# Performance work log

Measured on AMD Instinct MI355X. Metric: run time of the kernel, lower is better.

## Reference

```python
import jax, jax.numpy as jnp
import numpy as np

B, NPTS = 2, 60000
NX, NY = 256, 256
PCR0, PCR1 = -32.0, -32.0
PS0, PS1 = 0.25, 0.25
MAXPP = 32      # max points per pillar
MAXP = 12000    # max pillars
C = 64          # lidar_channels
SENT = NX * NY  # sentinel pillar id (> any valid id)
NEG = -1e9
EPS = 1e-5


def setup_inputs():
    key = jax.random.key(0)
    ks = jax.random.split(key, 16)
    xy = jax.random.uniform(ks[0], (B, NPTS, 2), minval=-34.0, maxval=34.0)
    z = jax.random.uniform(ks[1], (B, NPTS, 1), minval=-3.0, maxval=1.0)
    ir = jax.random.uniform(ks[2], (B, NPTS, 2))
    pts = jnp.concatenate([xy, z, ir], axis=-1).astype(jnp.float32)
    mask = jax.random.uniform(ks[3], (B, NPTS)) < 0.98

    def lin(k, i, o):
        return (jax.random.normal(k, (i, o)) / np.sqrt(i)).astype(jnp.float32)

    inp = {"lidar_points": pts, "lidar_mask": mask,
           "w1": lin(ks[4], 10, 64), "b1": 0.01 * jax.random.normal(ks[5], (64,), jnp.float32),
           "g1": jnp.ones(64, jnp.float32), "be1": jnp.zeros(64, jnp.float32),
           "w2": lin(ks[6], 64, 64), "b2": 0.01 * jax.random.normal(ks[7], (64,), jnp.float32),
           "g2": jnp.ones(64, jnp.float32), "be2": jnp.zeros(64, jnp.float32)}
    for i, n in enumerate(["1", "2", "3"]):
        inp["cw" + n] = (jax.random.normal(ks[8 + i], (64, 64, 3, 3)) / np.sqrt(64 * 9)).astype(jnp.float32)
        inp["cb" + n] = 0.01 * jax.random.normal(ks[11 + i], (64,), jnp.float32)
        inp["cg" + n] = jnp.ones(64, jnp.float32)
        inp["cbe" + n] = jnp.zeros(64, jnp.float32)
    return inp


def bn1d(x, g, b):  # training-mode BN over rows (biased var), matches torch BatchNorm1d forward
    m = x.mean(0)
    v = ((x - m) ** 2).mean(0)
    return (x - m) * jax.lax.rsqrt(v + EPS) * g + b


def bn2d(x, g, b):  # training-mode BN over (N,H,W) per channel
    m = x.mean((0, 2, 3), keepdims=True)
    v = ((x - m) ** 2).mean((0, 2, 3), keepdims=True)
    return (x - m) * jax.lax.rsqrt(v + EPS) * g[None, :, None, None] + b[None, :, None, None]


def conv3(x, w, b):
    y = jax.lax.conv_general_dilated(x, w, (1, 1), 'SAME',
                                     dimension_numbers=('NCHW', 'OIHW', 'NCHW'))
    return y + b[None, :, None, None]


def pillarize(pts, msk):
    """pts: (N,5) xyzir, msk: (N,) bool -> padded pillar tensors (fixed shapes)."""
    n = pts.shape[0]
    ix = jnp.clip(((pts[:, 0] - PCR0) / PS0).astype(jnp.int32), 0, NX - 1)
    iy = jnp.clip(((pts[:, 1] - PCR1) / PS1).astype(jnp.int32), 0, NY - 1)
    pid = jnp.where(msk, iy * NX + ix, SENT)
    # sorted unique ids; keep the first (smallest) MAXP, like torch.unique + truncation
    spid = jnp.sort(pid)
    is_new = jnp.concatenate([jnp.array([True]), spid[1:] != spid[:-1]])
    urank = jnp.cumsum(is_new) - 1
    dest = jnp.where(is_new & (urank < MAXP) & (spid < SENT), urank, MAXP)
    uids = jnp.full((MAXP + 1,), SENT, dtype=pid.dtype).at[dest].set(spid)[:MAXP]  # ascending, SENT-padded
    inv = jnp.clip(jnp.searchsorted(uids, pid), 0, MAXP - 1)
    valid = (uids[inv] == pid) & (pid < SENT)
    # rank of each point within its pillar, in original point order (stable sort)
    seg = jnp.where(valid, inv, MAXP)
    order = jnp.argsort(seg)  # stable
    sseg = seg[order]
    pos = jnp.arange(n)
    first = jnp.concatenate([jnp.array([True]), sseg[1:] != sseg[:-1]])
    start = jax.lax.cummax(jnp.where(first, pos, 0))
    rank = jnp.zeros(n, jnp.int32).at[order].set((pos - start).astype(jnp.int32))
    keep = valid & (rank < MAXPP)  # first MAXPP points per pillar (matches truncation-then-mean)
    seg2 = jnp.where(keep, inv, MAXP)  # dump slot = MAXP
    cnt = jnp.zeros(MAXP + 1, pts.dtype).at[seg2].add(1.0)
    sums = jnp.zeros((MAXP + 1, 3), pts.dtype).at[seg2].add(jnp.where(keep[:, None], pts[:, :3], 0.0))
    mean = sums / jnp.maximum(cnt, 1.0)[:, None]
    ctr = mean[seg2]  # per-point pillar centroid (over kept points)
    gx = PCR0 + ((pid % NX).astype(pts.dtype) + 0.5) * PS0
    gy = PCR1 + ((pid // NX).astype(pts.dtype) + 0.5) * PS1
    aug = jnp.concatenate([pts, pts[:, :3] - ctr, gx[:, None], gy[:, None]], axis=1)  # (N,10)
    rk = jnp.minimum(rank, MAXPP - 1)
    pf = jnp.zeros((MAXP + 1, MAXPP, 10), pts.dtype).at[seg2, rk].set(
        jnp.where(keep[:, None], aug, 0.0))[:MAXP]
    pm = jnp.zeros((MAXP + 1, MAXPP), bool).at[seg2, rk].set(keep)[:MAXP]
    pvalid = uids < SENT
    coords = jnp.where(pvalid[:, None], jnp.stack([uids % NX, uids // NX], axis=-1), 0)
    return pf, pm, coords, pvalid


def pillar_net(pf, pm, w1, b1, g1, be1, w2, b2, g2, be2):
    npil, pp, ci = pf.shape
    x = pf.reshape(npil * pp, ci) @ w1 + b1
    x = jax.nn.relu(bn1d(x, g1, be1))
    x = x @ w2 + b2
    x = jax.nn.relu(bn1d(x, g2, be2))
    x = x.reshape(npil, pp, -1)
    x = jnp.where(pm[:, :, None], x, NEG)
    return x.max(axis=1)  # (npil, C)


def reference(lidar_points, lidar_mask, w1, b1, g1, be1, w2, b2, g2, be2,
              cw1, cb1, cg1, cbe1, cw2, cb2, cg2, cbe2, cw3, cb3, cg3, cbe3):
    pf, pm, coords, pvalid = jax.vmap(pillarize)(lidar_points, lidar_mask)
    # pillar net is applied per batch element in the original loop -> per-sample BN stats
    feat = jax.vmap(lambda a, m: pillar_net(a, m, w1, b1, g1, be1, w2, b2, g2, be2))(pf, pm)
    lin = coords[..., 1] * NX + coords[..., 0]          # (B, MAXP)
    f = jnp.where(pvalid[..., None], feat, 0.0)          # padded pillars contribute nothing
    bev = jax.vmap(lambda l, ff: jnp.zeros((NY * NX, C), ff.dtype).at[l].add(ff))(lin, f)
    bev = bev.reshape(-1, NY, NX, C).transpose(0, 3, 1, 2)  # (B,C,NY,NX)
    x = jax.nn.relu(bn2d(conv3(bev, cw1, cb1), cg1, cbe1))
    x = jax.nn.relu(bn2d(conv3(x, cw2, cb2), cg2, cbe2))
    x = jax.nn.relu(bn2d(conv3(x, cw3, cb3), cg3, cbe3))
    return x
```

## Files before the change

kernel.cpp:

```cpp
#include <hip/hip_runtime.h>

#define NPTS 60000
#define NXG 256
#define NCELL 65536
#define MAXP 12000
#define MAXPP 32
#define NROWS (MAXP*MAXPP)

typedef float f32x32 __attribute__((ext_vector_type(32)));
typedef float f32x4  __attribute__((ext_vector_type(4)));
typedef short s16x8  __attribute__((ext_vector_type(8)));

__device__ __forceinline__ short to_bf16(float f){
  unsigned u = __float_as_uint(f);
  unsigned r = (u + 0x7FFFu + ((u>>16)&1u)) >> 16;
  return (short)r;
}

__global__ __launch_bounds__(256) void prep(uint4* __restrict__ p1, size_t n1,
                                            uint4* __restrict__ p2, size_t n2,
                                            const float* __restrict__ w0, const float* __restrict__ w1,
                                            const float* __restrict__ w2, short* __restrict__ wh){
  size_t idx = (size_t)blockIdx.x*256 + threadIdx.x;
  size_t stride = (size_t)gridDim.x*256;
  const uint4 z = make_uint4(0,0,0,0);
  for (size_t k=idx; k<n1; k+=stride) p1[k]=z;
  for (size_t k=idx; k<n2; k+=stride) p2[k]=z;
  for (size_t k=idx; k<3*36864; k+=stride){
    int l = (int)(k / 36864), r = (int)(k - (size_t)l*36864);
    const float* w = (l==0)? w0 : ((l==1)? w1 : w2);
    int ic = r & 63, oc = (r>>6)&63, tap = r>>12;
    wh[k] = to_bf16(w[(oc*64+ic)*9 + tap]);
  }
}

__global__ void compute_pid(const float* __restrict__ pts, const void* __restrict__ maskp,
                            int* __restrict__ pid, int* __restrict__ pptr,
                            int* __restrict__ ccnt){
  __shared__ int cf32, cbig;
  if (threadIdx.x==0){ cf32=0; cbig=0; }
  __syncthreads();
  {
    int lf=0, lb=0;
    const unsigned* mu = (const unsigned*)maskp;
    for (int k=0;k<4;k++){
      unsigned x = mu[threadIdx.x*4+k];
      if (x==0x3f800000u) lf++;
      else if (x>1u) lb++;
    }
    if (lf) atomicAdd(&cf32, lf);
    if (lb) atomicAdd(&cbig, lb);
  }
  __syncthreads();
  int mode = (cf32>64) ? 2 : ((cbig>0) ? 1 : 0);
  int i = blockIdx.x*blockDim.x + threadIdx.x;
  if (i>=NPTS) return;
  int b = blockIdx.y;
  int gi = b*NPTS+i;
  bool m;
  if (mode==0)      m = ((const int*)maskp)[gi]!=0;
  else if (mode==1) m = ((const unsigned char*)maskp)[gi]!=0;
  else              m = ((const float*)maskp)[gi]!=0.f;
  int cell = -1;
  if (m){
    float x = pts[(size_t)gi*5+0], y = pts[(size_t)gi*5+1];
    int ix = (int)((x - (-32.0f)) / 0.25f);
    ix = ix<0?0:(ix>255?255:ix);
    int iy = (int)((y - (-32.0f)) / 0.25f);
    iy = iy<0?0:(iy>255?255:iy);
    cell = iy*NXG + ix;
    atomicAdd(&ccnt[b*NCELL+cell], 1);
  }
  pid[gi] = cell;
  pptr[gi] = -1;
}

__global__ __launch_bounds__(256) void scan_a(const int* __restrict__ ccnt,
                                              int2* __restrict__ bpart){
  int b = blockIdx.y, blk = blockIdx.x, t = threadIdx.x;
  int4 v = *(const int4*)&ccnt[b*NCELL + blk*1024 + t*4];
  int occ = (v.x>0)+(v.y>0)+(v.z>0)+(v.w>0);
  int cnt = v.x+v.y+v.z+v.w;
  #pragma unroll
  for (int off=32; off>0; off>>=1){
    occ += __shfl_xor(occ, off, 64);
    cnt += __shfl_xor(cnt, off, 64);
  }
  __shared__ int so[4], sc[4];
  int wv = t>>6, lane = t&63;
  if (lane==0){ so[wv]=occ; sc[wv]=cnt; }
  __syncthreads();
  if (t==0) bpart[b*64+blk] = make_int2(so[0]+so[1]+so[2]+so[3], sc[0]+sc[1]+sc[2]+sc[3]);
}

__global__ __launch_bounds__(256) void scan_b(const int* __restrict__ ccnt,
    const int2* __restrict__ bpart,
    int* __restrict__ crank, int* __restrict__ cstart, int* __restrict__ pcell,
    int* __restrict__ misc, int* __restrict__ heavy){
  __shared__ int swo[4], swc[4], sk[4];
  __shared__ int bo_, bc_;
  int b = blockIdx.y, blk = blockIdx.x, t = threadIdx.x;
  int wv = t>>6, lane = t&63;
  if (t < 64){
    int2 p = bpart[b*64+t];
    int po = (t<blk)? p.x : 0;
    int pc = (t<blk)? p.y : 0;
    int to = p.x;
    int tc = p.y;
    #pragma unroll
    for (int off=32; off>0; off>>=1){
      po += __shfl_xor(po, off, 64);
      pc += __shfl_xor(pc, off, 64);
      to += __shfl_xor(to, off, 64);
      tc += __shfl_xor(tc, off, 64);
    }
    if (t==0){
      bo_ = po; bc_ = pc;
      if (blk==0){
        misc[1+b] = (to < MAXP) ? to : MAXP;
        misc[5+b] = tc;
      }
    }
  }
  int4 v = *(const int4*)&ccnt[b*NCELL + blk*1024 + t*4];
  int occ = (v.x>0)+(v.y>0)+(v.z>0)+(v.w>0);
  int cnt = v.x+v.y+v.z+v.w;
  int io = occ, ic = cnt;
  #pragma unroll
  for (int off=1; off<64; off<<=1){
    int ao = __shfl_up(io, off, 64);
    int ac = __shfl_up(ic, off, 64);
    if (lane >= off){ io += ao; ic += ac; }
  }
  if (lane==63){ swo[wv]=io; swc[wv]=ic; }
  __syncthreads();
  int wvo=0, wvc=0;
  #pragma unroll
  for (int w2=0; w2<4; w2++){
    if (w2<wv){ wvo += swo[w2]; wvc += swc[w2]; }
  }
  int eo = bo_ + wvo + io - occ;
  int ec = bc_ + wvc + ic - cnt;
  int kept = 0;
  int cellb = blk*1024 + t*4;
  int vv[4] = {v.x,v.y,v.z,v.w};
  #pragma unroll
  for (int j=0;j<4;j++){
    int c = cellb+j; int val = vv[j];
    if (val>0){
      crank[b*NCELL+c]=eo; cstart[b*NCELL+c]=ec;
      if (eo<MAXP){
        pcell[b*MAXP+eo]=c;
        kept += (val<MAXPP)? val : MAXPP;
        if (val>MAXPP){
          int hi = atomicAdd(&heavy[b],1);
          if (hi<64) heavy[2 + b*64 + hi] = c;
        }
      }
      eo++; ec+=val;
    }
  }
  #pragma unroll
  for (int off=32; off>0; off>>=1) kept += __shfl_xor(kept, off, 64);
  if (lane==0) sk[wv]=kept;
  __syncthreads();
  if (t==0) atomicAdd(&misc[3+b], sk[0]+sk[1]+sk[2]+sk[3]);
}

__global__ void scatter_points(const int* __restrict__ pid, const int* __restrict__ ccnt,
    const int* __restrict__ crank, const int* __restrict__ cstart,
    int* __restrict__ ctmp, int* __restrict__ plist, int* __restrict__ pptr){
  int i = blockIdx.x*blockDim.x + threadIdx.x;
  if (i>=NPTS) return;
  int b = blockIdx.y;
  int gi = b*NPTS+i;
  int cell = pid[gi];
  if (cell<0) return;
  int bc = b*NCELL+cell;
  int pos = cstart[bc] + atomicAdd(&ctmp[bc],1);
  plist[b*NPTS+pos] = i;
  int r = crank[bc];
  if (r>=0 && r<MAXP && ccnt[bc]<=MAXPP) pptr[gi] = r;
}

__global__ void heavy_select(const int* __restrict__ ccnt, const int* __restrict__ crank,
    const int* __restrict__ cstart, const int* __restrict__ plist,
    const int* __restrict__ heavy, int* __restrict__ pptr){
  int b = blockIdx.y;
  int hn = heavy[b]; if (hn>64) hn=64;
  if ((int)blockIdx.x >= hn) return;
  int cell = heavy[2 + b*64 + blockIdx.x];
  int bc = b*NCELL+cell;
  int cnt = ccnt[bc], start = cstart[bc], pr = crank[bc];
  for (int e=threadIdx.x; e<cnt; e+=blockDim.x){
    int pe = plist[b*NPTS+start+e];
    int rank=0;
    for (int k=0;k<cnt;k++) rank += (plist[b*NPTS+start+k] < pe);
    if (rank<MAXPP) pptr[b*NPTS+pe] = pr;
  }
}

__global__ __launch_bounds__(256) void gather_cpts(const float* __restrict__ pts,
    const int* __restrict__ pid, const int* __restrict__ pptr,
    const int* __restrict__ plist, const int* __restrict__ misc,
    float* __restrict__ cpts, float* __restrict__ psum){
  int pos = blockIdx.x*256 + threadIdx.x;
  int b = blockIdx.y;
  if (pos >= misc[5+b]) return;
  int i = plist[b*NPTS+pos];
  int gi = b*NPTS+i;
  const float* qp = &pts[(size_t)gi*5];
  float x=qp[0], y=qp[1], z=qp[2], i1=qp[3], i2=qp[4];
  int cell = pid[gi];
  int rid = pptr[gi];
  float gx = -32.0f + ((float)(cell&255)+0.5f)*0.25f;
  float gy = -32.0f + ((float)(cell>>8)+0.5f)*0.25f;
  float4* cp = (float4*)&cpts[(size_t)(b*NPTS+pos)*8];
  cp[0] = make_float4(x,y,z,i1);
  cp[1] = make_float4(i2,gx,gy,__int_as_float(rid));
  if (rid>=0){
    float* s = &psum[(size_t)(b*MAXP+rid)*4];
    atomicAdd(s+0,x); atomicAdd(s+1,y); atomicAdd(s+2,z); atomicAdd(s+3,1.f);
  }
}

#define MM_ACC(K,V) { if ((K)<32) m0[(K)&31]+=(V); else if ((K)<64) m1[((K)-32)&31]+=(V); else m2+=(V); }
__global__ __launch_bounds__(256) void moments(const float* __restrict__ cpts,
    const float* __restrict__ psum, const int* __restrict__ misc,
    float* __restrict__ lstat){
  int b = blockIdx.y;
  int n = misc[5+b];
  f32x32 m0, m1; float m2 = 0.f;
  #pragma unroll
  for (int j=0;j<32;j++){ m0[j]=0.f; m1[j]=0.f; }
  for (int pos = blockIdx.x*256+threadIdx.x; pos<n; pos += gridDim.x*256){
    const float4* cp = (const float4*)&cpts[(size_t)(b*NPTS+pos)*8];
    float4 f1 = cp[0], f2 = cp[1];
    int rid = __float_as_int(f2.w);
    if (rid<0) continue;
    float4 mc = *(const float4*)&psum[(size_t)(b*MAXP+rid)*4];
    float inv = 1.f/fmaxf(mc.w,1.f);
    float aug[10] = {f1.x,f1.y,f1.z,f1.w,f2.x,
                     f1.x-mc.x*inv, f1.y-mc.y*inv, f1.z-mc.z*inv, f2.y, f2.z};
    #pragma unroll
    for (int d=0; d<10; d++){
      #pragma unroll
      for (int e=d; e<10; e++){
        const int k = d*10 - d*(d-1)/2 + (e-d);
        MM_ACC(k, aug[d]*aug[e]);
      }
      const int kl = 55+d;
      MM_ACC(kl, aug[d]);
    }
  }
  int lane = threadIdx.x & 63;
  int rep = ((blockIdx.x*256+threadIdx.x)>>6) & 15;
  float* dst = &lstat[(size_t)(rep*2+b)*65];
  #pragma unroll
  for (int j=0;j<32;j++){
    float v = m0[j];
    #pragma unroll
    for (int off=32; off>0; off>>=1) v += __shfl_xor(v, off, 64);
    if (lane==0) atomicAdd(&dst[j], v);
  }
  #pragma unroll
  for (int j=0;j<32;j++){
    float v = m1[j];
    #pragma unroll
    for (int off=32; off>0; off>>=1) v += __shfl_xor(v, off, 64);
    if (lane==0) atomicAdd(&dst[32+j], v);
  }
  {
    float v = m2;
    #pragma unroll
    for (int off=32; off>0; off>>=1) v += __shfl_xor(v, off, 64);
    if (lane==0) atomicAdd(&dst[64], v);
  }
}

__global__ __launch_bounds__(256) void pillar_mlp(const float* __restrict__ cpts,
    const int* __restrict__ pcell, const int* __restrict__ cstart,
    const int* __restrict__ ccnt, const float* __restrict__ psum,
    const int* __restrict__ misc,
    const float* __restrict__ w1, const float* __restrict__ b1,
    const float* __restrict__ g1, const float* __restrict__ be1,
    const float* __restrict__ w2, const float* __restrict__ b2,
    const float* __restrict__ lstat, float* __restrict__ l2stat,
    float* __restrict__ fmx, float* __restrict__ fmn){
  __shared__ float sM[2][65];
  const int lane = threadIdx.x & 63;
  float w1c[10];
  #pragma unroll
  for (int d=0;d<10;d++) w1c[d] = w1[d*64+lane];
  for (int e=threadIdx.x; e<130; e+=256){
    int bb = e/65, k = e-bb*65;
    float s=0.f;
    for (int r=0;r<16;r++) s += lstat[(size_t)(r*2+bb)*65+k];
    sM[bb][k]=s;
  }
  __syncthreads();
  const float b1c = b1[lane], b2c = b2[lane];
  const float g1c = g1[lane], be1c = be1[lane];
  float sc1_0, sh1_0, sc1_1, sh1_1;
  #pragma unroll
  for (int bb=0;bb<2;bb++){
    float nk = (float)misc[3+bb];
    const float N = (float)NROWS;
    float pad = N - nk;
    float lw = 0.f;
    #pragma unroll
    for (int d=0;d<10;d++) lw += sM[bb][55+d]*w1c[d];
    float s = nk*b1c + lw;
    float qq = nk*b1c*b1c + 2.f*b1c*lw;
    #pragma unroll
    for (int d=0; d<10; d++){
      #pragma unroll
      for (int e=d; e<10; e++){
        float m = sM[bb][d*10 - d*(d-1)/2 + (e-d)];
        qq += ((d==e)?1.f:2.f)*m*w1c[d]*w1c[e];
      }
    }
    float St = s + pad*b1c;
    float Qt = qq + pad*b1c*b1c;
    float mu = St/N;
    float var = fmaxf(Qt/N - mu*mu, 0.f);
    float sc = g1c*rsqrtf(var+1e-5f);
    float sh = be1c-mu*sc;
    if (bb){ sc1_1=sc; sh1_1=sh; } else { sc1_0=sc; sh1_0=sh; }
  }
  f32x32 w2lo, w2hi;
  #pragma unroll
  for (int c=0;c<32;c++) w2lo[c] = w2[(size_t)c*64+lane];
  #pragma unroll
  for (int c=0;c<32;c++) w2hi[c] = w2[(size_t)(c+32)*64+lane];
  const int npil0 = misc[1], npil1 = misc[2];
  float s2_0=0.f, q2_0=0.f, s2_1=0.f, q2_1=0.f;

  const int wglobal = (blockIdx.x*256 + threadIdx.x) >> 6;
  const int nwaves = (gridDim.x*256) >> 6;
  for (int qq = wglobal; qq < 2*MAXP; qq += nwaves){
    int b = (qq >= MAXP) ? 1 : 0;
    int p = qq - b*MAXP;
    int npil = b ? npil1 : npil0;
    if (p >= npil) continue;
    int cell = pcell[b*MAXP+p];
    int bc = b*NCELL+cell;
    int cnt = ccnt[bc], start = cstart[bc];
    const float* mc = &psum[(size_t)(b*MAXP+p)*4];
    float minv = 1.f/fmaxf(mc[3],1.f);
    float mx = mc[0]*minv, my = mc[1]*minv, mz = mc[2]*minv;
    float gx = -32.0f + ((float)(cell&255)+0.5f)*0.25f;
    float gy = -32.0f + ((float)(cell>>8)+0.5f)*0.25f;
    float sc1 = b ? sc1_1 : sc1_0;
    float sh1 = b ? sh1_1 : sh1_0;
    float tmax = -1e30f, tmin = 1e30f;
    float s2 = 0.f, q2 = 0.f;
    for (int k=0; k<cnt; k++){
      const float4* cp = (const float4*)&cpts[(size_t)(b*NPTS+start+k)*8];
      float4 f1 = cp[0], f2 = cp[1];
      int rid = __float_as_int(f2.w);
      if (rid != p) continue;
      float x=f1.x, y=f1.y, z=f1.z, i1=f1.w, i2=f2.x;
      float acc = b1c;
      acc = fmaf(x, w1c[0], acc);
      acc = fmaf(y, w1c[1], acc);
      acc = fmaf(z, w1c[2], acc);
      acc = fmaf(i1, w1c[3], acc);
      acc = fmaf(i2, w1c[4], acc);
      acc = fmaf(x-mx, w1c[5], acc);
      acc = fmaf(y-my, w1c[6], acc);
      acc = fmaf(z-mz, w1c[7], acc);
      acc = fmaf(gx, w1c[8], acc);
      acc = fmaf(gy, w1c[9], acc);
      float zz = fmaxf(acc*sc1+sh1, 0.f);
      float t = b2c;
      #pragma unroll
      for (int c=0;c<32;c++){
        float zc = __int_as_float(__builtin_amdgcn_readlane(__float_as_int(zz), c));
        t = fmaf(zc, w2lo[c], t);
      }
      #pragma unroll
      for (int c=0;c<32;c++){
        float zc = __int_as_float(__builtin_amdgcn_readlane(__float_as_int(zz), c+32));
        t = fmaf(zc, w2hi[c], t);
      }
      tmax = fmaxf(tmax, t);
      tmin = fminf(tmin, t);
      s2 += t; q2 += t*t;
    }
    fmx[(size_t)(b*MAXP+p)*64 + lane] = tmax;
    fmn[(size_t)(b*MAXP+p)*64 + lane] = tmin;
    if (b){ s2_1 += s2; q2_1 += q2; } else { s2_0 += s2; q2_0 += q2; }
  }
  int rep = wglobal & 15;
  atomicAdd(&l2stat[((rep*2+0)*2+0)*64+lane], s2_0);
  atomicAdd(&l2stat[((rep*2+0)*2+1)*64+lane], q2_0);
  atomicAdd(&l2stat[((rep*2+1)*2+0)*64+lane], s2_1);
  atomicAdd(&l2stat[((rep*2+1)*2+1)*64+lane], q2_1);
}

__global__ void stats_fin2(const float* __restrict__ w1, const float* __restrict__ b1,
    const float* __restrict__ g1, const float* __restrict__ be1,
    const float* __restrict__ w2, const float* __restrict__ b2,
    const float* __restrict__ g2, const float* __restrict__ be2,
    const float* __restrict__ lstat, const float* __restrict__ l2stat,
    const int* __restrict__ misc, float* __restrict__ stats){
  __shared__ float M[65];
  __shared__ float z0s[64];
  int b = blockIdx.x, c = threadIdx.x;
  for (int e=c; e<65; e+=64){
    float s=0.f;
    for (int r=0;r<16;r++) s += lstat[(size_t)(r*2+b)*65+e];
    M[e]=s;
  }
  __syncthreads();
  float wcol[10];
  #pragma unroll
  for (int d=0;d<10;d++) wcol[d] = w1[d*64+c];
  float b1c = b1[c];
  float nk = (float)misc[3+b];
  const float N = (float)NROWS;
  float pad = N - nk;
  float lw = 0.f;
  #pragma unroll
  for (int d=0;d<10;d++) lw += M[55+d]*wcol[d];
  float s = nk*b1c + lw;
  float qq = nk*b1c*b1c + 2.f*b1c*lw;
  #pragma unroll
  for (int d=0; d<10; d++){
    #pragma unroll
    for (int e=d; e<10; e++){
      float m = M[d*10 - d*(d-1)/2 + (e-d)];
      qq += ((d==e)?1.f:2.f)*m*wcol[d]*wcol[e];
    }
  }
  float St = s + pad*b1c;
  float Qt = qq + pad*b1c*b1c;
  float mu = St/N;
  float var = fmaxf(Qt/N - mu*mu, 0.f);
  float sc1 = g1[c]*rsqrtf(var+1e-5f);
  float sh1 = be1[c]-mu*sc1;
  float z0 = fmaxf(b1c*sc1+sh1, 0.f);
  z0s[c]=z0;
  __syncthreads();
  float t0 = b2[c];
  for (int i2=0;i2<64;i2++) t0 += z0s[i2]*w2[(size_t)i2*64+c];
  float s2 = pad*t0, q2 = pad*t0*t0;
  for (int r=0;r<16;r++){
    s2 += l2stat[((r*2+b)*2+0)*64+c];
    q2 += l2stat[((r*2+b)*2+1)*64+c];
  }
  float m2 = s2/N;
  float v2 = fmaxf(q2/N - m2*m2, 0.f);
  float sc2 = g2[c]*rsqrtf(v2+1e-5f);
  float* S = &stats[(size_t)b*512];
  S[384+c]=sc2; S[448+c]=be2[c]-m2*sc2;
}

__global__ void scatter_bev(const float* __restrict__ fmx, const float* __restrict__ fmn,
                            const int* __restrict__ pcell, const int* __restrict__ misc,
                            const float* __restrict__ stats, short* __restrict__ bevh){
  int tid = blockIdx.x*256+threadIdx.x;
  if (tid >= 2*64*MAXP) return;
  int c = tid & 63;
  int bp = tid >> 6;
  int b = bp / MAXP;
  int p = bp - b*MAXP;
  if (p >= misc[1+b]) return;
  float sc2 = stats[(size_t)b*512+384+c], sh2 = stats[(size_t)b*512+448+c];
  float t = (sc2 >= 0.f) ? fmx[tid] : fmn[tid];
  float v = fmaxf(sc2*t+sh2, 0.f);
  int cell = pcell[b*MAXP+p];
  bevh[((size_t)((b<<16) + cell))*64 + c] = to_bf16(v);
}

#define MFMA16(A,B,C) __builtin_amdgcn_mfma_f32_16x16x32_bf16(A,B,C,0,0,0)

__global__ __launch_bounds__(512,4) void conv_mfma(const short* __restrict__ xh,
    const short* __restrict__ wh, const float* __restrict__ bias,
    const float* __restrict__ pstat, const float* __restrict__ pg, const float* __restrict__ pbe,
    short* __restrict__ outh, float* __restrict__ outf,
    float* __restrict__ stat){
  __shared__ short sX[324*40];
  __shared__ short sW[576*40];
  __shared__ float sBN[128];
  __shared__ float ss[64], sq[64];
  const int tX = blockIdx.x*16, tY = blockIdx.y*16;
  const int b = blockIdx.z;
  const int t = threadIdx.x;
  const int lane = t & 63, wv = t >> 6;
  const int colx = lane & 15;
  const int kb = (lane >> 4) * 8;
  const int ocb = (wv >> 2) * 32;
  const int ry  = (wv & 3) * 4;
  if (t < 64){ ss[t]=0.f; sq[t]=0.f; }
  if (t >= 64 && t < 128 && pstat){
    int c = t-64;
    const float n = 131072.f;
    float m = pstat[c]/n;
    float v = fmaxf(pstat[64+c]/n - m*m, 0.f);
    float sc = pg[c]*rsqrtf(v+1e-5f);
    sBN[c]=sc; sBN[64+c]=pbe[c]-m*sc;
  }

  f32x4 a00={0.f,0.f,0.f,0.f}, a01=a00, a02=a00, a03=a00;
  f32x4 a10=a00, a11=a00, a12=a00, a13=a00;

  for (int h=0; h<2; ++h){
    __syncthreads();
    for (int e=t; e<1296; e+=512){
      int px = e>>2, j = e&3;
      int yy = px/18, xx = px - yy*18;
      int gy = tY+yy-1, gx = tX+xx-1;
      uint4 v = make_uint4(0,0,0,0);
      if ((unsigned)gy<256u && (unsigned)gx<256u){
        v = *(const uint4*)&xh[((size_t)((b<<16) + (gy<<8) + gx))*64 + h*32 + j*8];
        if (pstat){
          unsigned arr[4] = {v.x, v.y, v.z, v.w};
          #pragma unroll
          for (int j2=0;j2<4;j2++){
            unsigned wrd = arr[j2];
            int ch = h*32 + j*8 + j2*2;
            float lo = __uint_as_float(wrd<<16);
            float hi = __uint_as_float(wrd & 0xffff0000u);
            lo = fmaxf(lo*sBN[ch]+sBN[64+ch], 0.f);
            hi = fmaxf(hi*sBN[ch+1]+sBN[64+ch+1], 0.f);
            arr[j2] = (unsigned)(unsigned short)to_bf16(lo) |
                      (((unsigned)(unsigned short)to_bf16(hi))<<16);
          }
          v = make_uint4(arr[0],arr[1],arr[2],arr[3]);
        }
      }
      *(uint4*)&sX[px*40 + j*8] = v;
    }
    for (int e=t; e<2304; e+=512){
      int row = e>>2, j = e&3;
      int tap = row>>6, oc = row&63;
      uint4 v = *(const uint4*)&wh[(size_t)tap*4096 + oc*64 + h*32 + j*8];
      *(uint4*)&sW[row*40 + j*8] = v;
    }
    __syncthreads();
    #pragma unroll
    for (int tap=0; tap<9; ++tap){
      const int dy = tap/3, dx = tap - dy*3;
      s16x8 wA = *(const s16x8*)&sW[(tap*64 + ocb +  0 + colx)*40 + kb];
      s16x8 wB = *(const s16x8*)&sW[(tap*64 + ocb + 16 + colx)*40 + kb];
      s16x8 x0 = *(const s16x8*)&sX[((ry+0+dy)*18 + colx+dx)*40 + kb];
      s16x8 x1 = *(const s16x8*)&sX[((ry+1+dy)*18 + colx+dx)*40 + kb];
      s16x8 x2 = *(const s16x8*)&sX[((ry+2+dy)*18 + colx+dx)*40 + kb];
      s16x8 x3 = *(const s16x8*)&sX[((ry+3+dy)*18 + colx+dx)*40 + kb];
      a00 = MFMA16(wA,x0,a00); a01 = MFMA16(wA,x1,a01);
      a02 = MFMA16(wA,x2,a02); a03 = MFMA16(wA,x3,a03);
      a10 = MFMA16(wB,x0,a10); a11 = MFMA16(wB,x1,a11);
      a12 = MFMA16(wB,x2,a12); a13 = MFMA16(wB,x3,a13);
    }
  }
  const int ocl = (lane>>4)*4;
  #define DOG(G, A0,A1,A2,A3) { \
    const int oc0g = ocb + G*16 + ocl; \
    float bj0=bias[oc0g], bj1=bias[oc0g+1], bj2=bias[oc0g+2], bj3=bias[oc0g+3]; \
    float v00=A0[0]+bj0, v01=A0[1]+bj1, v02=A0[2]+bj2, v03=A0[3]+bj3; \
    float v10=A1[0]+bj0, v11=A1[1]+bj1, v12=A1[2]+bj2, v13=A1[3]+bj3; \
    float v20=A2[0]+bj0, v21=A2[1]+bj1, v22=A2[2]+bj2, v23=A2[3]+bj3; \
    float v30=A3[0]+bj0, v31=A3[1]+bj1, v32=A3[2]+bj2, v33=A3[3]+bj3; \
    float s0=v00+v10+v20+v30, q0=v00*v00+v10*v10+v20*v20+v30*v30; \
    float s1=v01+v11+v21+v31, q1=v01*v01+v11*v11+v21*v21+v31*v31; \
    float s2=v02+v12+v22+v32, q2=v02*v02+v12*v12+v22*v22+v32*v32; \
    float s3=v03+v13+v23+v33, q3=v03*v03+v13*v13+v23*v23+v33*v33; \
    s0+=__shfl_xor(s0,1,64); s0+=__shfl_xor(s0,2,64); s0+=__shfl_xor(s0,4,64); s0+=__shfl_xor(s0,8,64); \
    q0+=__shfl_xor(q0,1,64); q0+=__shfl_xor(q0,2,64); q0+=__shfl_xor(q0,4,64); q0+=__shfl_xor(q0,8,64); \
    s1+=__shfl_xor(s1,1,64); s1+=__shfl_xor(s1,2,64); s1+=__shfl_xor(s1,4,64); s1+=__shfl_xor(s1,8,64); \
    q1+=__shfl_xor(q1,1,64); q1+=__shfl_xor(q1,2,64); q1+=__shfl_xor(q1,4,64); q1+=__shfl_xor(q1,8,64); \
    s2+=__shfl_xor(s2,1,64); s2+=__shfl_xor(s2,2,64); s2+=__shfl_xor(s2,4,64); s2+=__shfl_xor(s2,8,64); \
    q2+=__shfl_xor(q2,1,64); q2+=__shfl_xor(q2,2,64); q2+=__shfl_xor(q2,4,64); q2+=__shfl_xor(q2,8,64); \
    s3+=__shfl_xor(s3,1,64); s3+=__shfl_xor(s3,2,64); s3+=__shfl_xor(s3,4,64); s3+=__shfl_xor(s3,8,64); \
    q3+=__shfl_xor(q3,1,64); q3+=__shfl_xor(q3,2,64); q3+=__shfl_xor(q3,4,64); q3+=__shfl_xor(q3,8,64); \
    if (colx==0){ \
      atomicAdd(&ss[oc0g],s0);   atomicAdd(&sq[oc0g],q0); \
      atomicAdd(&ss[oc0g+1],s1); atomicAdd(&sq[oc0g+1],q1); \
      atomicAdd(&ss[oc0g+2],s2); atomicAdd(&sq[oc0g+2],q2); \
      atomicAdd(&ss[oc0g+3],s3); atomicAdd(&sq[oc0g+3],q3); \
    } \
    if (outh){ \
      size_t pb = (size_t)((b<<16) + tX + colx); \
      *(short4*)&outh[(pb + ((tY+ry+0)<<8))*64 + oc0g] = make_short4(to_bf16(v00),to_bf16(v01),to_bf16(v02),to_bf16(v03)); \
      *(short4*)&outh[(pb + ((tY+ry+1)<<8))*64 + oc0g] = make_short4(to_bf16(v10),to_bf16(v11),to_bf16(v12),to_bf16(v13)); \
      *(short4*)&outh[(pb + ((tY+ry+2)<<8))*64 + oc0g] = make_short4(to_bf16(v20),to_bf16(v21),to_bf16(v22),to_bf16(v23)); \
      *(short4*)&outh[(pb + ((tY+ry+3)<<8))*64 + oc0g] = make_short4(to_bf16(v30),to_bf16(v31),to_bf16(v32),to_bf16(v33)); \
    } else { \
      size_t cb0 = (((size_t)(b*64+oc0g))<<16) + ((tY+ry)<<8) + tX + colx; \
      outf[cb0          ] = v00; outf[cb0+(1<<16)      ] = v01; outf[cb0+(2<<16)      ] = v02; outf[cb0+(3<<16)      ] = v03; \
      outf[cb0+256      ] = v10; outf[cb0+(1<<16)+256  ] = v11; outf[cb0+(2<<16)+256  ] = v12; outf[cb0+(3<<16)+256  ] = v13; \
      outf[cb0+512      ] = v20; outf[cb0+(1<<16)+512  ] = v21; outf[cb0+(2<<16)+512  ] = v22; outf[cb0+(3<<16)+512  ] = v23; \
      outf[cb0+768      ] = v30; outf[cb0+(1<<16)+768  ] = v31; outf[cb0+(2<<16)+768  ] = v32; outf[cb0+(3<<16)+768  ] = v33; \
    } \
  }
  DOG(0, a00,a01,a02,a03)
  DOG(1, a10,a11,a12,a13)
  #undef DOG
  __syncthreads();
  if (t < 64){
    atomicAdd(&stat[t],    ss[t]);
    atomicAdd(&stat[64+t], sq[t]);
  }
}

__global__ __launch_bounds__(256) void bn_apply(float* __restrict__ x, const float* __restrict__ bnst,
                                                const float* __restrict__ g, const float* __restrict__ be){
  __shared__ float sBN[128];
  if (threadIdx.x < 64){
    int c = threadIdx.x;
    const float n = 131072.f;
    float m = bnst[c]/n;
    float v = fmaxf(bnst[64+c]/n - m*m, 0.f);
    float sc = g[c]*rsqrtf(v+1e-5f);
    sBN[c]=sc; sBN[64+c]=be[c]-m*sc;
  }
  __syncthreads();
  size_t idx = (size_t)blockIdx.x*256 + threadIdx.x;
  size_t stride = (size_t)gridDim.x*256;
  float4* p = (float4*)x;
  for (size_t k=idx; k<2097152ULL; k+=stride){
    int c = (int)((k>>14)&63);
    float sc = sBN[c], sh = sBN[64+c];
    float4 v = p[k];
    v.x=fmaxf(v.x*sc+sh,0.f); v.y=fmaxf(v.y*sc+sh,0.f);
    v.z=fmaxf(v.z*sc+sh,0.f); v.w=fmaxf(v.w*sc+sh,0.f);
    p[k]=v;
  }
}

extern "C" void kernel_launch(void* const* d_in, const int* in_sizes, int n_in,
                              void* d_out, int out_size, void* d_ws, size_t ws_size,
                              hipStream_t stream){
  const float* pts  = (const float*)d_in[0];
  const void*  mask = d_in[1];
  const float* w1 = (const float*)d_in[2];
  const float* b1 = (const float*)d_in[3];
  const float* g1 = (const float*)d_in[4];
  const float* be1= (const float*)d_in[5];
  const float* w2 = (const float*)d_in[6];
  const float* b2 = (const float*)d_in[7];
  const float* g2 = (const float*)d_in[8];
  const float* be2= (const float*)d_in[9];
  const float* cw[3]  = {(const float*)d_in[10],(const float*)d_in[14],(const float*)d_in[18]};
  const float* cb[3]  = {(const float*)d_in[11],(const float*)d_in[15],(const float*)d_in[19]};
  const float* cg[3]  = {(const float*)d_in[12],(const float*)d_in[16],(const float*)d_in[20]};
  const float* cbe[3] = {(const float*)d_in[13],(const float*)d_in[17],(const float*)d_in[21]};
  float* out = (float*)d_out;

  char* W = (char*)d_ws;
  size_t off = 0;
  auto A = [&](size_t n){ size_t r = off; off = (off + n + 255) & ~(size_t)255; return r; };
  short*    BIGH  = (short*)   (W + A((size_t)2*NCELL*64*2));
  short*    OUT1H = (short*)   (W + A((size_t)2*NCELL*64*2));
  int*      PID   = (int*)     (W + A((size_t)2*NPTS*4));
  int*      CRANK = (int*)     (W + A((size_t)2*NCELL*4));
  int*      CSTART= (int*)     (W + A((size_t)2*NCELL*4));
  int*      PLIST = (int*)     (W + A((size_t)2*NPTS*4));
  int*      PPTR  = (int*)     (W + A((size_t)2*NPTS*4));
  int*      PCELL = (int*)     (W + A((size_t)2*MAXP*4));
  float*    CPTS  = (float*)   (W + A((size_t)2*NPTS*8*4));
  float*    FMX   = (float*)   (W + A((size_t)2*MAXP*64*4));
  float*    FMN   = (float*)   (W + A((size_t)2*MAXP*64*4));
  short*    WH    = (short*)   (W + A((size_t)3*36864*2));
  int2*     BPART = (int2*)    (W + A((size_t)2*64*8));
  size_t zbeg = off;
  int*      CCNT  = (int*)     (W + A((size_t)2*NCELL*4));
  int*      CTMP  = (int*)     (W + A((size_t)2*NCELL*4));
  float*    PSUM  = (float*)   (W + A((size_t)2*MAXP*16));
  float*    STATS = (float*)   (W + A((size_t)2*512*4));
  float*    LSTAT = (float*)   (W + A((size_t)16*2*65*4));
  float*    L2STAT= (float*)   (W + A((size_t)16*2*2*64*4));
  float*    BNST  = (float*)   (W + A((size_t)3*256*4));
  int*      HEAVY = (int*)     (W + A((size_t)(2+2*64)*4));
  int*      MISC  = (int*)     (W + A(256));
  size_t zend = off;

  prep<<<2048,256,0,stream>>>((uint4*)BIGH, (size_t)2*NCELL*64*2/16,
                              (uint4*)(W+zbeg), (zend-zbeg)/16,
                              cw[0], cw[1], cw[2], WH);

  dim3 perPt((NPTS+255)/256, 2);

  compute_pid<<<perPt,256,0,stream>>>(pts, mask, PID, PPTR, CCNT);
  scan_a<<<dim3(64,2),256,0,stream>>>(CCNT, BPART);
  scan_b<<<dim3(64,2),256,0,stream>>>(CCNT, BPART, CRANK, CSTART, PCELL, MISC, HEAVY);
  scatter_points<<<perPt,256,0,stream>>>(PID, CCNT, CRANK, CSTART, CTMP, PLIST, PPTR);
  heavy_select<<<dim3(64,2),64,0,stream>>>(CCNT, CRANK, CSTART, PLIST, HEAVY, PPTR);
  gather_cpts<<<perPt,256,0,stream>>>(pts, PID, PPTR, PLIST, MISC, CPTS, PSUM);
  moments<<<dim3(120,2),256,0,stream>>>(CPTS, PSUM, MISC, LSTAT);
  pillar_mlp<<<2048,256,0,stream>>>(CPTS, PCELL, CSTART, CCNT, PSUM, MISC,
                                    w1, b1, g1, be1, w2, b2, LSTAT, L2STAT, FMX, FMN);
  stats_fin2<<<2,64,0,stream>>>(w1, b1, g1, be1, w2, b2, g2, be2, LSTAT, L2STAT, MISC, STATS);
  scatter_bev<<<(2*64*MAXP+255)/256,256,0,stream>>>(FMX, FMN, PCELL, MISC, STATS, BIGH);

  conv_mfma<<<dim3(16,16,2),512,0,stream>>>(BIGH, WH, cb[0], nullptr, nullptr, nullptr,
                                            OUT1H, nullptr, BNST);
  conv_mfma<<<dim3(16,16,2),512,0,stream>>>(OUT1H, WH+36864, cb[1], BNST, cg[0], cbe[0],
                                            BIGH, nullptr, BNST+256);
  conv_mfma<<<dim3(16,16,2),512,0,stream>>>(BIGH, WH+2*36864, cb[2], BNST+256, cg[1], cbe[1],
                                            nullptr, out, BNST+512);
  bn_apply<<<2048,256,0,stream>>>(out, BNST+512, cg[2], cbe[2]);
}
```

Before: 220.3 us.

## Split pillar MLP into per-point bf16 MFMA kernel and pillar max reduction

Replaces the per-pillar scalar FMA/readlane MLP with a point-major kernel that runs both linear layers on 16x16x32 bf16 MFMA tiles and stages the hidden activations through LDS. The results go to a new per-point float buffer, and a separate pillar_max kernel reduces them per pillar into max, min and BN2 statistics. The aim is to move the dense 64x64 matmul onto matrix cores and get rid of the serial readlane chain. In exchange it adds a global write and read of about 30 MB of intermediate data, one more kernel launch, and bf16 rounding of the inputs, weights and hidden activations. The grid-cell coordinate features are now read from cpts fields instead of being recomputed per pillar.

```diff
diff --git a/kernel.cpp b/kernel.cpp
--- a/kernel.cpp
+++ b/kernel.cpp
@@ -20,7 +20,9 @@
 __global__ __launch_bounds__(256) void prep(uint4* __restrict__ p1, size_t n1,
                                             uint4* __restrict__ p2, size_t n2,
                                             const float* __restrict__ w0, const float* __restrict__ w1,
-                                            const float* __restrict__ w2, short* __restrict__ wh){
+                                            const float* __restrict__ w2, short* __restrict__ wh,
+                                            const float* __restrict__ mw1, const float* __restrict__ mw2,
+                                            short* __restrict__ w1h, short* __restrict__ w2h){
   size_t idx = (size_t)blockIdx.x*256 + threadIdx.x;
   size_t stride = (size_t)gridDim.x*256;
   const uint4 z = make_uint4(0,0,0,0);
@@ -32,6 +34,12 @@
     int ic = r & 63, oc = (r>>6)&63, tap = r>>12;
     wh[k] = to_bf16(w[(oc*64+ic)*9 + tap]);
   }
+  for (size_t k=idx; k<2048; k+=stride){
+    int kk = (int)(k>>6), oc = (int)(k&63);
+    w1h[k] = (kk<10) ? to_bf16(mw1[kk*64+oc]) : (short)0;
+  }
+  for (size_t k=idx; k<4096; k+=stride)
+    w2h[k] = to_bf16(mw2[k]);
 }
 
 __global__ void compute_pid(const float* __restrict__ pts, const void* __restrict__ maskp,
@@ -278,64 +286,145 @@
   }
 }
 
-__global__ __launch_bounds__(256) void pillar_mlp(const float* __restrict__ cpts,
-    const int* __restrict__ pcell, const int* __restrict__ cstart,
-    const int* __restrict__ ccnt, const float* __restrict__ psum,
-    const int* __restrict__ misc,
+#define MFMA16(A,B,C) __builtin_amdgcn_mfma_f32_16x16x32_bf16(A,B,C,0,0,0)
+
+__global__ __launch_bounds__(256) void point_mlp(const float* __restrict__ cpts,
+    const float* __restrict__ psum, const int* __restrict__ misc,
     const float* __restrict__ w1, const float* __restrict__ b1,
     const float* __restrict__ g1, const float* __restrict__ be1,
-    const float* __restrict__ w2, const float* __restrict__ b2,
-    const float* __restrict__ lstat, float* __restrict__ l2stat,
-    float* __restrict__ fmx, float* __restrict__ fmn){
-  __shared__ float sM[2][65];
-  const int lane = threadIdx.x & 63;
-  float w1c[10];
-  #pragma unroll
-  for (int d=0;d<10;d++) w1c[d] = w1[d*64+lane];
-  for (int e=threadIdx.x; e<130; e+=256){
-    int bb = e/65, k = e-bb*65;
+    const short* __restrict__ w1h, const short* __restrict__ w2h,
+    const float* __restrict__ lstat, float* __restrict__ tbuf){
+  __shared__ float sM[65];
+  __shared__ float sBN1[128];
+  __shared__ short zT[4][16*72];
+  const int b = blockIdx.y;
+  const int t = threadIdx.x;
+  for (int e=t; e<65; e+=256){
     float s=0.f;
-    for (int r=0;r<16;r++) s += lstat[(size_t)(r*2+bb)*65+k];
-    sM[bb][k]=s;
-  }
-  __syncthreads();
-  const float b1c = b1[lane], b2c = b2[lane];
-  const float g1c = g1[lane], be1c = be1[lane];
-  float sc1_0, sh1_0, sc1_1, sh1_1;
-  #pragma unroll
-  for (int bb=0;bb<2;bb++){
-    float nk = (float)misc[3+bb];
+    for (int r=0;r<16;r++) s += lstat[(size_t)(r*2+b)*65+e];
+    sM[e]=s;
+  }
+  __syncthreads();
+  if (t < 64){
+    int c = t;
+    float wcol[10];
+    #pragma unroll
+    for (int d=0;d<10;d++) wcol[d] = w1[d*64+c];
+    float b1c = b1[c];
+    float nk = (float)misc[3+b];
     const float N = (float)NROWS;
     float pad = N - nk;
     float lw = 0.f;
     #pragma unroll
-    for (int d=0;d<10;d++) lw += sM[bb][55+d]*w1c[d];
+    for (int d=0;d<10;d++) lw += sM[55+d]*wcol[d];
     float s = nk*b1c + lw;
     float qq = nk*b1c*b1c + 2.f*b1c*lw;
     #pragma unroll
     for (int d=0; d<10; d++){
       #pragma unroll
       for (int e=d; e<10; e++){
-        float m = sM[bb][d*10 - d*(d-1)/2 + (e-d)];
-        qq += ((d==e)?1.f:2.f)*m*w1c[d]*w1c[e];
+        float m = sM[d*10 - d*(d-1)/2 + (e-d)];
+        qq += ((d==e)?1.f:2.f)*m*wcol[d]*wcol[e];
       }
     }
     float St = s + pad*b1c;
     float Qt = qq + pad*b1c*b1c;
     float mu = St/N;
     float var = fmaxf(Qt/N - mu*mu, 0.f);
-    float sc = g1c*rsqrtf(var+1e-5f);
-    float sh = be1c-mu*sc;
-    if (bb){ sc1_1=sc; sh1_1=sh; } else { sc1_0=sc; sh1_0=sh; }
-  }
-  f32x32 w2lo, w2hi;
-  #pragma unroll
-  for (int c=0;c<32;c++) w2lo[c] = w2[(size_t)c*64+lane];
-  #pragma unroll
-  for (int c=0;c<32;c++) w2hi[c] = w2[(size_t)(c+32)*64+lane];
+    float sc = g1[c]*rsqrtf(var+1e-5f);
+    float sh = be1[c]-mu*sc;
+    sBN1[c]=sc; sBN1[64+c]=b1c*sc+sh;
+  }
+  __syncthreads();
+  const int lane = t & 63, wv = t >> 6;
+  const int colx = lane & 15;
+  const int kq = lane >> 4, kb = kq*8;
+  s16x8 w1f0, w1f1, w1f2, w1f3;
+  s16x8 a2f0, a2f1, a2f2, a2f3;
+  s16x8 b2f0, b2f1, b2f2, b2f3;
+  #pragma unroll
+  for (int j=0;j<8;j++){
+    w1f0[j]=w1h[(kb+j)*64 +  0+colx]; w1f1[j]=w1h[(kb+j)*64 + 16+colx];
+    w1f2[j]=w1h[(kb+j)*64 + 32+colx]; w1f3[j]=w1h[(kb+j)*64 + 48+colx];
+    a2f0[j]=w2h[(kb+j)*64 +  0+colx]; a2f1[j]=w2h[(kb+j)*64 + 16+colx];
+    a2f2[j]=w2h[(kb+j)*64 + 32+colx]; a2f3[j]=w2h[(kb+j)*64 + 48+colx];
+    b2f0[j]=w2h[(32+kb+j)*64 +  0+colx]; b2f1[j]=w2h[(32+kb+j)*64 + 16+colx];
+    b2f2[j]=w2h[(32+kb+j)*64 + 32+colx]; b2f3[j]=w2h[(32+kb+j)*64 + 48+colx];
+  }
+  float sc1v0=sBN1[colx],    sh1v0=sBN1[64+colx];
+  float sc1v1=sBN1[16+colx], sh1v1=sBN1[80+colx];
+  float sc1v2=sBN1[32+colx], sh1v2=sBN1[96+colx];
+  float sc1v3=sBN1[48+colx], sh1v3=sBN1[112+colx];
+  const int n = misc[5+b];
+  const int ntiles = (n+15)>>4;
+  short* myZ = zT[wv];
+  for (int tile = blockIdx.x*4 + wv; tile < ntiles; tile += gridDim.x*4){
+    int pos0 = tile*16;
+    int pos = pos0 + colx;
+    float aug[10];
+    #pragma unroll
+    for (int d=0;d<10;d++) aug[d]=0.f;
+    if (pos < n){
+      const float4* cp = (const float4*)&cpts[(size_t)(b*NPTS+pos)*8];
+      float4 f1 = cp[0], f2 = cp[1];
+      int rid = __float_as_int(f2.w);
+      int ridc = (rid>=0)? rid : 0;
+      float4 mc = *(const float4*)&psum[(size_t)(b*MAXP+ridc)*4];
+      float inv = 1.f/fmaxf(mc.w,1.f);
+      aug[0]=f1.x; aug[1]=f1.y; aug[2]=f1.z; aug[3]=f1.w; aug[4]=f2.x;
+      aug[5]=f1.x-mc.x*inv; aug[6]=f1.y-mc.y*inv; aug[7]=f1.z-mc.z*inv;
+      aug[8]=f2.y; aug[9]=f2.z;
+    }
+    s16x8 af;
+    #pragma unroll
+    for (int j=0;j<8;j++){
+      float v = 0.f;
+      if (kq==0) v = aug[j];
+      else if (kq==1 && j<2) v = aug[8+j];
+      af[j] = to_bf16(v);
+    }
+    f32x4 y0={0.f,0.f,0.f,0.f}, y1=y0, y2=y0, y3=y0;
+    y0 = MFMA16(af, w1f0, y0);
+    y1 = MFMA16(af, w1f1, y1);
+    y2 = MFMA16(af, w1f2, y2);
+    y3 = MFMA16(af, w1f3, y3);
+    #pragma unroll
+    for (int m=0;m<4;m++){
+      int pr = (kq*4+m)*72;
+      myZ[pr +  0+colx] = to_bf16(fmaxf(y0[m]*sc1v0+sh1v0, 0.f));
+      myZ[pr + 16+colx] = to_bf16(fmaxf(y1[m]*sc1v1+sh1v1, 0.f));
+      myZ[pr + 32+colx] = to_bf16(fmaxf(y2[m]*sc1v2+sh1v2, 0.f));
+      myZ[pr + 48+colx] = to_bf16(fmaxf(y3[m]*sc1v3+sh1v3, 0.f));
+    }
+    s16x8 az0 = *(const s16x8*)&myZ[colx*72 + kb];
+    s16x8 az1 = *(const s16x8*)&myZ[colx*72 + 32 + kb];
+    f32x4 t0={0.f,0.f,0.f,0.f}, t1=t0, t2=t0, t3=t0;
+    t0 = MFMA16(az0, a2f0, t0); t0 = MFMA16(az1, b2f0, t0);
+    t1 = MFMA16(az0, a2f1, t1); t1 = MFMA16(az1, b2f1, t1);
+    t2 = MFMA16(az0, a2f2, t2); t2 = MFMA16(az1, b2f2, t2);
+    t3 = MFMA16(az0, a2f3, t3); t3 = MFMA16(az1, b2f3, t3);
+    #pragma unroll
+    for (int m=0;m<4;m++){
+      int pm = pos0 + kq*4 + m;
+      if (pm < n){
+        float* dst = &tbuf[(size_t)(b*NPTS+pm)*64];
+        dst[ 0+colx] = t0[m];
+        dst[16+colx] = t1[m];
+        dst[32+colx] = t2[m];
+        dst[48+colx] = t3[m];
+      }
+    }
+  }
+}
+
+__global__ __launch_bounds__(256) void pillar_max(const float* __restrict__ tbuf,
+    const float* __restrict__ cpts,
+    const int* __restrict__ pcell, const int* __restrict__ cstart,
+    const int* __restrict__ ccnt, const int* __restrict__ misc,
+    float* __restrict__ l2stat, float* __restrict__ fmx, float* __restrict__ fmn){
+  const int lane = threadIdx.x & 63;
   const int npil0 = misc[1], npil1 = misc[2];
   float s2_0=0.f, q2_0=0.f, s2_1=0.f, q2_1=0.f;
-
   const int wglobal = (blockIdx.x*256 + threadIdx.x) >> 6;
   const int nwaves = (gridDim.x*256) >> 6;
   for (int qq = wglobal; qq < 2*MAXP; qq += nwaves){
@@ -346,47 +435,16 @@
     int cell = pcell[b*MAXP+p];
     int bc = b*NCELL+cell;
     int cnt = ccnt[bc], start = cstart[bc];
-    const float* mc = &psum[(size_t)(b*MAXP+p)*4];
-    float minv = 1.f/fmaxf(mc[3],1.f);
-    float mx = mc[0]*minv, my = mc[1]*minv, mz = mc[2]*minv;
-    float gx = -32.0f + ((float)(cell&255)+0.5f)*0.25f;
-    float gy = -32.0f + ((float)(cell>>8)+0.5f)*0.25f;
-    float sc1 = b ? sc1_1 : sc1_0;
-    float sh1 = b ? sh1_1 : sh1_0;
     float tmax = -1e30f, tmin = 1e30f;
     float s2 = 0.f, q2 = 0.f;
     for (int k=0; k<cnt; k++){
-      const float4* cp = (const float4*)&cpts[(size_t)(b*NPTS+start+k)*8];
-      float4 f1 = cp[0], f2 = cp[1];
-      int rid = __float_as_int(f2.w);
-      if (rid != p) continue;
-      float x=f1.x, y=f1.y, z=f1.z, i1=f1.w, i2=f2.x;
-      float acc = b1c;
-      acc = fmaf(x, w1c[0], acc);
-      acc = fmaf(y, w1c[1], acc);
-      acc = fmaf(z, w1c[2], acc);
-      acc = fmaf(i1, w1c[3], acc);
-      acc = fmaf(i2, w1c[4], acc);
-      acc = fmaf(x-mx, w1c[5], acc);
-      acc = fmaf(y-my, w1c[6], acc);
-      acc = fmaf(z-mz, w1c[7], acc);
-      acc = fmaf(gx, w1c[8], acc);
-      acc = fmaf(gy, w1c[9], acc);
-      float zz = fmaxf(acc*sc1+sh1, 0.f);
-      float t = b2c;
-      #pragma unroll
-      for (int c=0;c<32;c++){
-        float zc = __int_as_float(__builtin_amdgcn_readlane(__float_as_int(zz), c));
-        t = fmaf(zc, w2lo[c], t);
+      int rid = __float_as_int(cpts[(size_t)(b*NPTS+start+k)*8 + 7]);
+      float tv = tbuf[(size_t)(b*NPTS+start+k)*64 + lane];
+      if (rid == p){
+        tmax = fmaxf(tmax, tv);
+        tmin = fminf(tmin, tv);
+        s2 += tv; q2 += tv*tv;
       }
-      #pragma unroll
-      for (int c=0;c<32;c++){
-        float zc = __int_as_float(__builtin_amdgcn_readlane(__float_as_int(zz), c+32));
-        t = fmaf(zc, w2hi[c], t);
-      }
-      tmax = fmaxf(tmax, t);
-      tmin = fminf(tmin, t);
-      s2 += t; q2 += t*t;
     }
     fmx[(size_t)(b*MAXP+p)*64 + lane] = tmax;
     fmn[(size_t)(b*MAXP+p)*64 + lane] = tmin;
@@ -473,8 +531,6 @@
   int cell = pcell[b*MAXP+p];
   bevh[((size_t)((b<<16) + cell))*64 + c] = to_bf16(v);
 }
-
-#define MFMA16(A,B,C) __builtin_amdgcn_mfma_f32_16x16x32_bf16(A,B,C,0,0,0)
 
 __global__ __launch_bounds__(512,4) void conv_mfma(const short* __restrict__ xh,
     const short* __restrict__ wh, const float* __restrict__ bias,
@@ -661,9 +717,12 @@
   int*      PPTR  = (int*)     (W + A((size_t)2*NPTS*4));
   int*      PCELL = (int*)     (W + A((size_t)2*MAXP*4));
   float*    CPTS  = (float*)   (W + A((size_t)2*NPTS*8*4));
+  float*    TBUF  = (float*)   (W + A((size_t)2*NPTS*64*4));
   float*    FMX   = (float*)   (W + A((size_t)2*MAXP*64*4));
   float*    FMN   = (float*)   (W + A((size_t)2*MAXP*64*4));
   short*    WH    = (short*)   (W + A((size_t)3*36864*2));
+  short*    W1H   = (short*)   (W + A((size_t)2048*2));
+  short*    W2H   = (short*)   (W + A((size_t)4096*2));
   int2*     BPART = (int2*)    (W + A((size_t)2*64*8));
   size_t zbeg = off;
   int*      CCNT  = (int*)     (W + A((size_t)2*NCELL*4));
@@ -679,7 +738,7 @@
 
   prep<<<2048,256,0,stream>>>((uint4*)BIGH, (size_t)2*NCELL*64*2/16,
                               (uint4*)(W+zbeg), (zend-zbeg)/16,
-                              cw[0], cw[1], cw[2], WH);
+                              cw[0], cw[1], cw[2], WH, w1, w2, W1H, W2H);
 
   dim3 perPt((NPTS+255)/256, 2);
 
@@ -690,8 +749,10 @@
   heavy_select<<<dim3(64,2),64,0,stream>>>(CCNT, CRANK, CSTART, PLIST, HEAVY, PPTR);
   gather_cpts<<<perPt,256,0,stream>>>(pts, PID, PPTR, PLIST, MISC, CPTS, PSUM);
   moments<<<dim3(120,2),256,0,stream>>>(CPTS, PSUM, MISC, LSTAT);
-  pillar_mlp<<<2048,256,0,stream>>>(CPTS, PCELL, CSTART, CCNT, PSUM, MISC,
-                                    w1, b1, g1, be1, w2, b2, LSTAT, L2STAT, FMX, FMN);
+  point_mlp<<<dim3(128,2),256,0,stream>>>(CPTS, PSUM, MISC, w1, b1, g1, be1,
+                                          W1H, W2H, LSTAT, TBUF);
+  pillar_max<<<2048,256,0,stream>>>(TBUF, CPTS, PCELL, CSTART, CCNT, MISC,
+                                    L2STAT, FMX, FMN);
   stats_fin2<<<2,64,0,stream>>>(w1, b1, g1, be1, w2, b2, g2, be2, LSTAT, L2STAT, MISC, STATS);
   scatter_bev<<<(2*64*MAXP+255)/256,256,0,stream>>>(FMX, FMN, PCELL, MISC, STATS, BIGH);
 
```

New measurement: 230.7 us. 1.05x slower.
